# Kernel tuning notes

Hardware: AMD Instinct MI355X
Metric: run time of the kernel (lower is better)

The kernel has to match this reference:

```python
import jax, jax.numpy as jnp
import numpy as np

B, N, DIN, DOUT, E, K = 64, 883, 2, 64, 10, 2
CIN = DIN + DOUT


def _dgcn(x, node_emb, time, day, speed, occupy,
          fc1_w, fc1_b, fc2_w, fc2_b, fc3_w, fc3_b, wpool, bpool):
    # x: (B, N, C); node_emb: (N, E); time/day/speed/occupy: (B, N, E)
    n = x.shape[1]
    # hyper-network filter from input features
    h = jax.nn.sigmoid(x @ fc1_w + fc1_b)
    h = jax.nn.sigmoid(h @ fc2_w + fc2_b)
    filt = h @ fc3_w + fc3_b                                  # (B, N, E)
    # dynamic node embedding: static emb modulated by time/day/speed/occupy embeddings
    dyn = node_emb[None] * time * day * speed * occupy        # (B, N, E)
    nodevec = jnp.tanh(dyn * filt)                            # (B, N, E)
    A = jax.nn.relu(jnp.einsum('bne,bme->bnm', nodevec, nodevec))  # (B, N, N)
    d = jnp.sum(A, axis=-1) ** -0.5                           # (B, N)
    I = jnp.eye(n, dtype=x.dtype)
    L = I[None] - A * d[:, :, None] * d[:, None, :]           # normalized laplacian support
    # cheb_k = 2 supports: identity and L
    x_g = jnp.stack([x, jnp.einsum('bnm,bmc->bnc', L, x)], axis=2)  # (B, N, K, C)
    weights = jnp.einsum('ne,ekio->nkio', node_emb, wpool)    # (N, K, C, O)
    bias = node_emb @ bpool                                   # (N, O)
    return jnp.einsum('bnki,nkio->bno', x_g, weights) + bias[None]


def setup_inputs() -> dict:
    key = jax.random.key(0)
    ks = jax.random.split(key, 23)
    rn = lambda k, s, sc=1.0: jax.random.normal(k, s, dtype=jnp.float32) * sc
    return dict(
        x=rn(ks[0], (B, N, DIN)),
        state=rn(ks[1], (B, N, DOUT), 0.1),
        node_embeddings=rn(ks[2], (N, E)),
        time=rn(ks[3], (B, N, E), 0.5),
        day=rn(ks[4], (B, N, E), 0.5),
        speed=rn(ks[5], (B, N, E), 0.5),
        occupy=rn(ks[6], (B, N, E), 0.5),
        gate_wpool=rn(ks[7], (E, K, CIN, 2 * DOUT), 0.1),
        gate_bpool=rn(ks[8], (E, 2 * DOUT), 0.1),
        gate_fc1_w=rn(ks[9], (CIN, 16), 0.1), gate_fc1_b=rn(ks[10], (16,), 0.1),
        gate_fc2_w=rn(ks[11], (16, 2), 0.1), gate_fc2_b=rn(ks[12], (2,), 0.1),
        gate_fc3_w=rn(ks[13], (2, E), 0.1), gate_fc3_b=rn(ks[14], (E,), 0.1),
        update_wpool=rn(ks[15], (E, K, CIN, DOUT), 0.1),
        update_bpool=rn(ks[16], (E, DOUT), 0.1),
        update_fc1_w=rn(ks[17], (CIN, 16), 0.1), update_fc1_b=rn(ks[18], (16,), 0.1),
        update_fc2_w=rn(ks[19], (16, 2), 0.1), update_fc2_b=rn(ks[20], (2,), 0.1),
        update_fc3_w=rn(ks[21], (2, E), 0.1), update_fc3_b=rn(ks[22], (E,), 0.1),
    )


def reference(x, state, node_embeddings, time, day, speed, occupy,
              gate_wpool, gate_bpool, gate_fc1_w, gate_fc1_b, gate_fc2_w,
              gate_fc2_b, gate_fc3_w, gate_fc3_b,
              update_wpool, update_bpool, update_fc1_w, update_fc1_b,
              update_fc2_w, update_fc2_b, update_fc3_w, update_fc3_b):
    xs = jnp.concatenate([x, state], axis=-1)                 # (B, N, DIN+DOUT)
    z_r = jax.nn.sigmoid(_dgcn(xs, node_embeddings, time, day, speed, occupy,
                               gate_fc1_w, gate_fc1_b, gate_fc2_w, gate_fc2_b,
                               gate_fc3_w, gate_fc3_b, gate_wpool, gate_bpool))
    z, r = jnp.split(z_r, 2, axis=-1)
    cand = jnp.concatenate([x, z * state], axis=-1)
    hc = jnp.tanh(_dgcn(cand, node_embeddings, time, day, speed, occupy,
                        update_fc1_w, update_fc1_b, update_fc2_w, update_fc2_b,
                        update_fc3_w, update_fc3_b, update_wpool, update_bpool))
    return r * state + (1.0 - r) * hc
```

## Files before the change

### kernel.cpp

```cpp
#include <hip/hip_runtime.h>
#include <cmath>

#define BB 64
#define NN 883
#define NP 896
#define EE 10
#define CC 66
#define KP 160
#define NT16 56
#define MB32 28

typedef __attribute__((ext_vector_type(8))) short bf16x8;
typedef __attribute__((ext_vector_type(4))) float f32x4;

__device__ __forceinline__ float sigmoidf_(float v) { return 1.f / (1.f + expf(-v)); }

__device__ __forceinline__ unsigned short f2bf(float f) {
  unsigned int u = __float_as_uint(f);
  u = u + 0x7FFFu + ((u >> 16) & 1u);
  return (unsigned short)(u >> 16);
}
__device__ __forceinline__ float bf2f(unsigned short h) {
  return __uint_as_float(((unsigned int)h) << 16);
}
__device__ __forceinline__ unsigned int pkrelu(float a, float b) {
  return (unsigned int)f2bf(fmaxf(a, 0.f)) | ((unsigned int)f2bf(fmaxf(b, 0.f)) << 16);
}


template<int PHASE>
__global__ __launch_bounds__(256) void k1_hyper(
    const float* __restrict__ x, const float* __restrict__ state,
    const float* __restrict__ zr, const float* __restrict__ emb,
    const float* __restrict__ tme, const float* __restrict__ day,
    const float* __restrict__ spd, const float* __restrict__ occ,
    const float* __restrict__ w1, const float* __restrict__ b1,
    const float* __restrict__ w2, const float* __restrict__ b2,
    const float* __restrict__ w3, const float* __restrict__ b3,
    unsigned short* __restrict__ Acat, unsigned short* __restrict__ nv2) {
  int idx = blockIdx.x * 256 + threadIdx.x;
  if (idx >= BB * NP) return;
  int b = idx / NP, n = idx - b * NP;
  size_t slot = ((size_t)(b * NT16 + (n >> 4)) * 32 + (n & 15) * 2) * 8;
  if (n >= NN) {
    *(uint4*)&nv2[slot] = make_uint4(0, 0, 0, 0);
    *(uint4*)&nv2[slot + 8] = make_uint4(0, 0, 0, 0);
    return;
  }
  int bn = b * NN + n;

  float xsr[CC];
  xsr[0] = x[bn * 2 + 0];
  xsr[1] = x[bn * 2 + 1];
#pragma unroll
  for (int j = 0; j < 64; ++j) {
    float s = state[bn * 64 + j];
    if (PHASE == 1) s *= zr[(size_t)bn * 128 + j];
    xsr[2 + j] = s;
  }
  {
    unsigned short a16[80];
#pragma unroll
    for (int c = 0; c < CC; ++c) a16[c] = f2bf(xsr[c]);
#pragma unroll
    for (int c = CC; c < 80; ++c) a16[c] = 0;
#pragma unroll
    for (int k = 0; k < 10; ++k) {
      unsigned int q0 = (unsigned int)a16[8 * k + 0] | ((unsigned int)a16[8 * k + 1] << 16);
      unsigned int q1 = (unsigned int)a16[8 * k + 2] | ((unsigned int)a16[8 * k + 3] << 16);
      unsigned int q2 = (unsigned int)a16[8 * k + 4] | ((unsigned int)a16[8 * k + 5] << 16);
      unsigned int q3 = (unsigned int)a16[8 * k + 6] | ((unsigned int)a16[8 * k + 7] << 16);
      *(uint4*)&Acat[(size_t)bn * KP + 8 * k] = make_uint4(q0, q1, q2, q3);
    }
  }

  float h1[16];
#pragma unroll
  for (int j = 0; j < 16; ++j) h1[j] = b1[j];
#pragma unroll
  for (int i = 0; i < CC; ++i) {
    float xv = xsr[i];
#pragma unroll
    for (int j = 0; j < 16; ++j) h1[j] = fmaf(xv, w1[i * 16 + j], h1[j]);
  }
#pragma unroll
  for (int j = 0; j < 16; ++j) h1[j] = sigmoidf_(h1[j]);

  float h2[2];
#pragma unroll
  for (int j = 0; j < 2; ++j) {
    float s = b2[j];
#pragma unroll
    for (int i = 0; i < 16; ++i) s = fmaf(h1[i], w2[i * 2 + j], s);
    h2[j] = sigmoidf_(s);
  }

  unsigned short nv16[16];
#pragma unroll
  for (int e = 0; e < EE; ++e) {
    float f = b3[e] + h2[0] * w3[e] + h2[1] * w3[EE + e];
    int be = bn * EE + e;
    float dyn = emb[n * EE + e] * tme[be] * day[be] * spd[be] * occ[be];
    nv16[e] = f2bf(tanhf(dyn * f));
  }
#pragma unroll
  for (int e = EE; e < 16; ++e) nv16[e] = 0;
  unsigned int w[8];
#pragma unroll
  for (int k = 0; k < 8; ++k)
    w[k] = (unsigned int)nv16[2 * k] | ((unsigned int)nv16[2 * k + 1] << 16);
  *(uint4*)&nv2[slot]     = make_uint4(w[0], w[1], w[2], w[3]);
  *(uint4*)&nv2[slot + 8] = make_uint4(w[4], w[5], w[6], w[7]);
}

__global__ __launch_bounds__(256) void k2_deg(const unsigned short* __restrict__ nv2,
                                              const unsigned short* __restrict__ Acat,
                                              float* __restrict__ d_g,
                                              unsigned short* __restrict__ xsd2) {
  int nt = blockIdx.x, b = blockIdx.y;
  int t = threadIdx.x, wid = t >> 6, lane = t & 63;
  int col = lane & 15, q = lane >> 4;
  __shared__ float tile[64][67];
  __shared__ float d_s[64];

  const unsigned short* nvb = nv2 + (size_t)b * NT16 * 32 * 8;
  bf16x8 zf = {0, 0, 0, 0, 0, 0, 0, 0};
  bf16x8 anv = zf;
  if (q < 2) anv = *(const bf16x8*)&nvb[((size_t)(nt * 4 + wid) * 32 + col * 2 + q) * 8];

  float rs[4] = {0.f, 0.f, 0.f, 0.f};
  bf16x8 cur = zf, nxt = zf;
  if (q < 2) cur = *(const bf16x8*)&nvb[((size_t)0 * 32 + col * 2 + q) * 8];
  for (int mt = 0; mt < NT16; ++mt) {
    if (q < 2 && mt + 1 < NT16)
      nxt = *(const bf16x8*)&nvb[((size_t)(mt + 1) * 32 + col * 2 + q) * 8];
    f32x4 z = {0.f, 0.f, 0.f, 0.f};
    f32x4 g = __builtin_amdgcn_mfma_f32_16x16x32_bf16(anv, cur, z, 0, 0, 0);
#pragma unroll
    for (int r = 0; r < 4; ++r) rs[r] += fmaxf(g[r], 0.f);
    cur = nxt;
  }
#pragma unroll
  for (int off = 1; off < 16; off <<= 1) {
#pragma unroll
    for (int r = 0; r < 4; ++r) rs[r] += __shfl_xor(rs[r], off);
  }
  if (col == 0) {
#pragma unroll
    for (int r = 0; r < 4; ++r) {
      int n = nt * 64 + wid * 16 + q * 4 + r;
      float dv = (n < NN) ? rsqrtf(rs[r]) : 0.f;
      d_g[b * NP + n] = dv;
      d_s[wid * 16 + q * 4 + r] = dv;
    }
  }
  __syncthreads();

  int mb = nt * 64;
  for (int idx = t; idx < 64 * CC; idx += 256) {
    int ml = idx / CC, c = idx - ml * CC;
    int m = mb + ml;
    float v = 0.f;
    if (m < NN) v = bf2f(Acat[((size_t)(b * NN + m)) * KP + c]);
    tile[ml][c] = v * d_s[ml];
  }
  __syncthreads();
  for (int idx = t; idx < 2 * 5 * 4 * 16; idx += 256) {
    int colw = idx & 15;
    int qw = (idx >> 4) & 3;
    int ctw = (idx >> 6) % 5;
    int mbbl = idx / (16 * 4 * 5);
    unsigned int o[4];
#pragma unroll
    for (int jj = 0; jj < 4; ++jj) {
      int ml = mbbl * 32 + qw * 8 + jj * 2;
      int c = ctw * 16 + colw;
      float v0 = (c < CC) ? tile[ml][c] : 0.f;
      float v1 = (c < CC) ? tile[ml + 1][c] : 0.f;
      o[jj] = (unsigned int)f2bf(v0) | ((unsigned int)f2bf(v1) << 16);
    }
    size_t dst = (((((size_t)b * MB32 + (nt * 2 + mbbl)) * 5 + ctw) * 4 + qw) * 16 + colw) * 8;
    *(uint4*)&xsd2[dst] = make_uint4(o[0], o[1], o[2], o[3]);
  }
}

__global__ __launch_bounds__(256) void k3_agg(const unsigned short* __restrict__ nv2,
                                              const float* __restrict__ d_g,
                                              const unsigned short* __restrict__ xsd2,
                                              unsigned short* __restrict__ Acat) {
  int nt = blockIdx.x, b = blockIdx.y, t = threadIdx.x;
  int wid = t >> 6, lane = t & 63, col = lane & 15, q = lane >> 4;
  int n16 = nt * 64 + wid * 16;

  const unsigned short* nvb = nv2 + (size_t)b * NT16 * 32 * 8;
  const unsigned short* xb = xsd2 + (size_t)b * MB32 * 5 * 4 * 16 * 8;

  bf16x8 zf = {0, 0, 0, 0, 0, 0, 0, 0};
  bf16x8 anv = zf;
  if (q < 2) anv = *(const bf16x8*)&nvb[((size_t)(nt * 4 + wid) * 32 + col * 2 + q) * 8];

  f32x4 acc[5];
#pragma unroll
  for (int ct = 0; ct < 5; ++ct) acc[ct] = (f32x4){0.f, 0.f, 0.f, 0.f};

  int base = ((q & 1) << 5) + col;
  bool hi = (q >= 2);

  for (int i = 0; i < MB32; ++i) {
    bf16x8 b0 = zf, b1 = zf;
    if (q < 2) {
      b0 = *(const bf16x8*)&nvb[((size_t)(i * 2) * 32 + col * 2 + q) * 8];
      b1 = *(const bf16x8*)&nvb[((size_t)(i * 2 + 1) * 32 + col * 2 + q) * 8];
    }
    bf16x8 xf[5];
#pragma unroll
    for (int ct = 0; ct < 5; ++ct)
      xf[ct] = *(const bf16x8*)&xb[((((size_t)i * 5 + ct) * 4 + q) * 16 + col) * 8];

    f32x4 z = {0.f, 0.f, 0.f, 0.f};
    f32x4 g0 = __builtin_amdgcn_mfma_f32_16x16x32_bf16(b0, anv, z, 0, 0, 0);
    f32x4 g1 = __builtin_amdgcn_mfma_f32_16x16x32_bf16(b1, anv, z, 0, 0, 0);
    unsigned int p00 = pkrelu(g0[0], g0[1]), p01 = pkrelu(g0[2], g0[3]);
    unsigned int p10 = pkrelu(g1[0], g1[1]), p11 = pkrelu(g1[2], g1[3]);
    unsigned int s00 = (unsigned int)__shfl((int)p00, base);
    unsigned int s01 = (unsigned int)__shfl((int)p01, base);
    unsigned int s02 = (unsigned int)__shfl((int)p00, base + 16);
    unsigned int s03 = (unsigned int)__shfl((int)p01, base + 16);
    unsigned int s10 = (unsigned int)__shfl((int)p10, base);
    unsigned int s11 = (unsigned int)__shfl((int)p11, base);
    unsigned int s12 = (unsigned int)__shfl((int)p10, base + 16);
    unsigned int s13 = (unsigned int)__shfl((int)p11, base + 16);
    union { unsigned int u[4]; bf16x8 v; } cv;
    cv.u[0] = hi ? s10 : s00;
    cv.u[1] = hi ? s11 : s01;
    cv.u[2] = hi ? s12 : s02;
    cv.u[3] = hi ? s13 : s03;

#pragma unroll
    for (int ct = 0; ct < 5; ++ct)
      acc[ct] = __builtin_amdgcn_mfma_f32_16x16x32_bf16(cv.v, xf[ct], acc[ct], 0, 0, 0);
  }

  float dn[4];
#pragma unroll
  for (int r = 0; r < 4; ++r) dn[r] = d_g[b * NP + n16 + q * 4 + r];
#pragma unroll
  for (int ct = 0; ct < 5; ++ct) {
    int c = ct * 16 + col;
#pragma unroll
    for (int r = 0; r < 4; ++r) {
      int n = n16 + q * 4 + r;
      if (n < NN)
        Acat[((size_t)(b * NN) + n) * KP + 80 + c] = f2bf(-(acc[ct][r] * dn[r]));
    }
  }
}

template<int OT, bool GATE>
__global__ __launch_bounds__(256) void k4b_gemm(
    const float* __restrict__ emb, const float* __restrict__ wpool,
    const float* __restrict__ bpool, const unsigned short* __restrict__ Acat,
    float* __restrict__ zr_w,
    const float* __restrict__ state, const float* __restrict__ zr_r,
    float* __restrict__ out) {
  int n = blockIdx.x, t = threadIdx.x;
  __shared__ __align__(16) unsigned short Ws[OT * 168];
  __shared__ float bias_s[OT];

  const int OG = OT / 4;
  int og = t % OG, ti = t / OG;
  int o4 = og * 4;
  float em[EE];
#pragma unroll
  for (int e = 0; e < EE; ++e) em[e] = emb[n * EE + e];

  for (int i = ti; i < CC; i += 256 / OG) {
    float4 s0 = make_float4(0.f, 0.f, 0.f, 0.f);
    float4 s1 = make_float4(0.f, 0.f, 0.f, 0.f);
#pragma unroll
    for (int e = 0; e < EE; ++e) {
      float4 w0 = *(const float4*)&wpool[(((size_t)(e * 2 + 0) * CC + i)) * OT + o4];
      float4 w1 = *(const float4*)&wpool[(((size_t)(e * 2 + 1) * CC + i)) * OT + o4];
      s0.x = fmaf(em[e], w0.x, s0.x); s0.y = fmaf(em[e], w0.y, s0.y);
      s0.z = fmaf(em[e], w0.z, s0.z); s0.w = fmaf(em[e], w0.w, s0.w);
      s1.x = fmaf(em[e], w1.x, s1.x); s1.y = fmaf(em[e], w1.y, s1.y);
      s1.z = fmaf(em[e], w1.z, s1.z); s1.w = fmaf(em[e], w1.w, s1.w);
    }
    Ws[(o4 + 0) * 168 + i] = f2bf(s0.x + s1.x);
    Ws[(o4 + 1) * 168 + i] = f2bf(s0.y + s1.y);
    Ws[(o4 + 2) * 168 + i] = f2bf(s0.z + s1.z);
    Ws[(o4 + 3) * 168 + i] = f2bf(s0.w + s1.w);
    Ws[(o4 + 0) * 168 + 80 + i] = f2bf(s1.x);
    Ws[(o4 + 1) * 168 + 80 + i] = f2bf(s1.y);
    Ws[(o4 + 2) * 168 + 80 + i] = f2bf(s1.z);
    Ws[(o4 + 3) * 168 + 80 + i] = f2bf(s1.w);
  }
  for (int idx = t; idx < OT * 14; idx += 256) {
    int o = idx / 14, kk = idx - o * 14;
    Ws[o * 168 + 66 + kk] = 0;
    Ws[o * 168 + 146 + kk] = 0;
  }
  if (t < OT) {
    float s = 0.f;
#pragma unroll
    for (int e = 0; e < EE; ++e) s = fmaf(em[e], bpool[e * OT + t], s);
    bias_s[t] = s;
  }
  __syncthreads();

  int wid = t >> 6, lane = t & 63, col = lane & 15, q = lane >> 4;
  int bA = wid * 16 + col;
  f32x4 acc[OT / 16];
#pragma unroll
  for (int ot = 0; ot < OT / 16; ++ot) acc[ot] = (f32x4){0.f, 0.f, 0.f, 0.f};

#pragma unroll
  for (int ks = 0; ks < 5; ++ks) {
    bf16x8 af = *(const bf16x8*)&Acat[((size_t)(bA * NN + n)) * KP + ks * 32 + q * 8];
#pragma unroll
    for (int ot = 0; ot < OT / 16; ++ot) {
      bf16x8 bf = *(const bf16x8*)&Ws[(ot * 16 + col) * 168 + ks * 32 + q * 8];
      acc[ot] = __builtin_amdgcn_mfma_f32_16x16x32_bf16(af, bf, acc[ot], 0, 0, 0);
    }
  }

#pragma unroll
  for (int ot = 0; ot < OT / 16; ++ot) {
    int o = ot * 16 + col;
    float bia = bias_s[o];
#pragma unroll
    for (int r = 0; r < 4; ++r) {
      int bb = wid * 16 + q * 4 + r;
      float v = acc[ot][r] + bia;
      if (GATE) {
        zr_w[((size_t)(bb * NN + n)) * 128 + o] = sigmoidf_(v);
      } else {
        float hc = tanhf(v);
        float rr = zr_r[((size_t)(bb * NN + n)) * 128 + 64 + o];
        float st = state[((size_t)(bb * NN + n)) * 64 + o];
        out[((size_t)(bb * NN + n)) * 64 + o] = fmaf(rr, st - hc, hc);
      }
    }
  }
}

extern "C" void kernel_launch(void* const* d_in, const int* in_sizes, int n_in,
                              void* d_out, int out_size, void* d_ws, size_t ws_size,
                              hipStream_t stream) {
  const float* x     = (const float*)d_in[0];
  const float* state = (const float*)d_in[1];
  const float* emb   = (const float*)d_in[2];
  const float* tme   = (const float*)d_in[3];
  const float* day   = (const float*)d_in[4];
  const float* spd   = (const float*)d_in[5];
  const float* occ   = (const float*)d_in[6];
  const float* gwp   = (const float*)d_in[7];
  const float* gbp   = (const float*)d_in[8];
  const float* gw1   = (const float*)d_in[9];
  const float* gb1   = (const float*)d_in[10];
  const float* gw2   = (const float*)d_in[11];
  const float* gb2   = (const float*)d_in[12];
  const float* gw3   = (const float*)d_in[13];
  const float* gb3   = (const float*)d_in[14];
  const float* uwp   = (const float*)d_in[15];
  const float* ubp   = (const float*)d_in[16];
  const float* uw1   = (const float*)d_in[17];
  const float* ub1   = (const float*)d_in[18];
  const float* uw2   = (const float*)d_in[19];
  const float* ub2   = (const float*)d_in[20];
  const float* uw3   = (const float*)d_in[21];
  const float* ub3   = (const float*)d_in[22];

  char* w = (char*)d_ws;
  unsigned short* Acat = (unsigned short*)w;  w += (size_t)BB * NN * KP * 2;
  unsigned short* nv2  = (unsigned short*)w;  w += (size_t)BB * NT16 * 32 * 8 * 2;
  unsigned short* xsd2 = (unsigned short*)w;  w += (size_t)BB * MB32 * 5 * 4 * 16 * 8 * 2;
  float* d_g  = (float*)w;  w += (size_t)BB * NP * 4;
  float* zr   = (float*)w;  w += (size_t)BB * NN * 128 * 4;

  dim3 b256(256);
  dim3 gK1((BB * NP) / 256);
  dim3 gK2(14, BB);
  dim3 gK4(NN);

  k1_hyper<0><<<gK1, b256, 0, stream>>>(x, state, zr, emb, tme, day, spd, occ,
                                        gw1, gb1, gw2, gb2, gw3, gb3, Acat, nv2);
  k2_deg<<<gK2, b256, 0, stream>>>(nv2, Acat, d_g, xsd2);
  k3_agg<<<gK2, b256, 0, stream>>>(nv2, d_g, xsd2, Acat);
  k4b_gemm<128, true><<<gK4, b256, 0, stream>>>(emb, gwp, gbp, Acat, zr,
                                                nullptr, nullptr, nullptr);
  k1_hyper<1><<<gK1, b256, 0, stream>>>(x, state, zr, emb, tme, day, spd, occ,
                                        uw1, ub1, uw2, ub2, uw3, ub3, Acat, nv2);
  k2_deg<<<gK2, b256, 0, stream>>>(nv2, Acat, d_g, xsd2);
  k3_agg<<<gK2, b256, 0, stream>>>(nv2, d_g, xsd2, Acat);
  k4b_gemm<64, false><<<gK4, b256, 0, stream>>>(emb, uwp, ubp, Acat, nullptr,
                                                state, zr, (float*)d_out);
}
```

Baseline: 355.1 us.

## Precompute per-node bf16 weights in separate kernel, stream them into GEMM

Adds a k4a_wprep kernel that builds the per-node weights (node_emb x wpool) in bf16, already in MFMA fragment order, into a workspace buffer. The gemm kernel then loads its B fragments straight from global memory and no longer builds them in shared memory with a __syncthreads. The per-node bias is now computed in registers in the epilogue. This takes the redundant per-block weight synthesis and its barrier off the gemm's critical path. The cost is an extra kernel launch and a large global weight buffer (about NN*8*160*16 bf16 elements) that is written and read back.

New measurement: 370.9 us. 4.4% more time.

```diff
diff --git a/kernel.cpp b/kernel.cpp
--- a/kernel.cpp
+++ b/kernel.cpp
@@ -256,78 +256,85 @@
   }
 }
 
+template<int OT>
+__global__ __launch_bounds__(160) void k4a_wprep(const float* __restrict__ emb,
+                                                 const float* __restrict__ wpool,
+                                                 unsigned short* __restrict__ Wg) {
+  const int OTILES = OT / 16;
+  int k = threadIdx.x;
+  int col = blockIdx.x & 15;
+  int ot = blockIdx.x >> 4;
+  int nc = blockIdx.y;
+  int o = ot * 16 + col;
+  int ks = k >> 5, qw = (k >> 3) & 3, j = k & 7;
+
+  int i = -1, half = 0;
+  if (k < CC) { i = k; half = 0; }
+  else if (k >= 80 && k < 80 + CC) { i = k - 80; half = 1; }
+
+  float wv[EE];
+#pragma unroll
+  for (int e = 0; e < EE; ++e) {
+    float v = 0.f;
+    if (i >= 0) {
+      v = wpool[(((size_t)(e * 2 + 1) * CC + i)) * OT + o];
+      if (half == 0) v += wpool[(((size_t)(e * 2 + 0) * CC + i)) * OT + o];
+    }
+    wv[e] = v;
+  }
+
+  __shared__ float emb_s[112 * EE];
+  int n0 = nc * 111;
+  int cnt = min(111, NN - n0);
+  for (int idx = k; idx < cnt * EE; idx += 160) emb_s[idx] = emb[n0 * EE + idx];
+  __syncthreads();
+
+  size_t wo = (((size_t)ot * 5 + ks) * 4 + qw) * 16 * 8 + col * 8 + j;
+  for (int nl = 0; nl < cnt; ++nl) {
+    float s = 0.f;
+#pragma unroll
+    for (int e = 0; e < EE; ++e) s = fmaf(emb_s[nl * EE + e], wv[e], s);
+    Wg[(size_t)(n0 + nl) * (OTILES * KP * 16) + wo] = f2bf(s);
+  }
+}
+
 template<int OT, bool GATE>
 __global__ __launch_bounds__(256) void k4b_gemm(
-    const float* __restrict__ emb, const float* __restrict__ wpool,
+    const float* __restrict__ emb, const unsigned short* __restrict__ Wg,
     const float* __restrict__ bpool, const unsigned short* __restrict__ Acat,
     float* __restrict__ zr_w,
     const float* __restrict__ state, const float* __restrict__ zr_r,
     float* __restrict__ out) {
+  const int OTILES = OT / 16;
   int n = blockIdx.x, t = threadIdx.x;
-  __shared__ __align__(16) unsigned short Ws[OT * 168];
-  __shared__ float bias_s[OT];
-
-  const int OG = OT / 4;
-  int og = t % OG, ti = t / OG;
-  int o4 = og * 4;
-  float em[EE];
-#pragma unroll
-  for (int e = 0; e < EE; ++e) em[e] = emb[n * EE + e];
-
-  for (int i = ti; i < CC; i += 256 / OG) {
-    float4 s0 = make_float4(0.f, 0.f, 0.f, 0.f);
-    float4 s1 = make_float4(0.f, 0.f, 0.f, 0.f);
-#pragma unroll
-    for (int e = 0; e < EE; ++e) {
-      float4 w0 = *(const float4*)&wpool[(((size_t)(e * 2 + 0) * CC + i)) * OT + o4];
-      float4 w1 = *(const float4*)&wpool[(((size_t)(e * 2 + 1) * CC + i)) * OT + o4];
-      s0.x = fmaf(em[e], w0.x, s0.x); s0.y = fmaf(em[e], w0.y, s0.y);
-      s0.z = fmaf(em[e], w0.z, s0.z); s0.w = fmaf(em[e], w0.w, s0.w);
-      s1.x = fmaf(em[e], w1.x, s1.x); s1.y = fmaf(em[e], w1.y, s1.y);
-      s1.z = fmaf(em[e], w1.z, s1.z); s1.w = fmaf(em[e], w1.w, s1.w);
-    }
-    Ws[(o4 + 0) * 168 + i] = f2bf(s0.x + s1.x);
-    Ws[(o4 + 1) * 168 + i] = f2bf(s0.y + s1.y);
-    Ws[(o4 + 2) * 168 + i] = f2bf(s0.z + s1.z);
-    Ws[(o4 + 3) * 168 + i] = f2bf(s0.w + s1.w);
-    Ws[(o4 + 0) * 168 + 80 + i] = f2bf(s1.x);
-    Ws[(o4 + 1) * 168 + 80 + i] = f2bf(s1.y);
-    Ws[(o4 + 2) * 168 + 80 + i] = f2bf(s1.z);
-    Ws[(o4 + 3) * 168 + 80 + i] = f2bf(s1.w);
-  }
-  for (int idx = t; idx < OT * 14; idx += 256) {
-    int o = idx / 14, kk = idx - o * 14;
-    Ws[o * 168 + 66 + kk] = 0;
-    Ws[o * 168 + 146 + kk] = 0;
-  }
-  if (t < OT) {
-    float s = 0.f;
-#pragma unroll
-    for (int e = 0; e < EE; ++e) s = fmaf(em[e], bpool[e * OT + t], s);
-    bias_s[t] = s;
-  }
-  __syncthreads();
-
   int wid = t >> 6, lane = t & 63, col = lane & 15, q = lane >> 4;
   int bA = wid * 16 + col;
-  f32x4 acc[OT / 16];
-#pragma unroll
-  for (int ot = 0; ot < OT / 16; ++ot) acc[ot] = (f32x4){0.f, 0.f, 0.f, 0.f};
+  const unsigned short* wb = Wg + (size_t)n * (OTILES * KP * 16);
+
+  f32x4 acc[OTILES];
+#pragma unroll
+  for (int ot = 0; ot < OTILES; ++ot) acc[ot] = (f32x4){0.f, 0.f, 0.f, 0.f};
 
 #pragma unroll
   for (int ks = 0; ks < 5; ++ks) {
     bf16x8 af = *(const bf16x8*)&Acat[((size_t)(bA * NN + n)) * KP + ks * 32 + q * 8];
 #pragma unroll
-    for (int ot = 0; ot < OT / 16; ++ot) {
-      bf16x8 bf = *(const bf16x8*)&Ws[(ot * 16 + col) * 168 + ks * 32 + q * 8];
+    for (int ot = 0; ot < OTILES; ++ot) {
+      bf16x8 bf = *(const bf16x8*)&wb[((((size_t)ot * 5 + ks) * 4 + q) * 16 + col) * 8];
       acc[ot] = __builtin_amdgcn_mfma_f32_16x16x32_bf16(af, bf, acc[ot], 0, 0, 0);
     }
   }
 
-#pragma unroll
-  for (int ot = 0; ot < OT / 16; ++ot) {
+  float em[EE];
+#pragma unroll
+  for (int e = 0; e < EE; ++e) em[e] = emb[n * EE + e];
+
+#pragma unroll
+  for (int ot = 0; ot < OTILES; ++ot) {
     int o = ot * 16 + col;
-    float bia = bias_s[o];
+    float bia = 0.f;
+#pragma unroll
+    for (int e = 0; e < EE; ++e) bia = fmaf(em[e], bpool[e * OT + o], bia);
 #pragma unroll
     for (int r = 0; r < 4; ++r) {
       int bb = wid * 16 + q * 4 + r;
@@ -377,22 +384,26 @@
   unsigned short* xsd2 = (unsigned short*)w;  w += (size_t)BB * MB32 * 5 * 4 * 16 * 8 * 2;
   float* d_g  = (float*)w;  w += (size_t)BB * NP * 4;
   float* zr   = (float*)w;  w += (size_t)BB * NN * 128 * 4;
-
-  dim3 b256(256);
+  unsigned short* Wg = (unsigned short*)w;  w += (size_t)NN * 8 * KP * 16 * 2;
+
+  dim3 b256(256), b160(160);
   dim3 gK1((BB * NP) / 256);
   dim3 gK2(14, BB);
   dim3 gK4(NN);
-
+  dim3 gWg(8 * 16, 8), gWu(4 * 16, 8);
+
+  k4a_wprep<128><<<gWg, b160, 0, stream>>>(emb, gwp, Wg);
   k1_hyper<0><<<gK1, b256, 0, stream>>>(x, state, zr, emb, tme, day, spd, occ,
                                         gw1, gb1, gw2, gb2, gw3, gb3, Acat, nv2);
   k2_deg<<<gK2, b256, 0, stream>>>(nv2, Acat, d_g, xsd2);
   k3_agg<<<gK2, b256, 0, stream>>>(nv2, d_g, xsd2, Acat);
-  k4b_gemm<128, true><<<gK4, b256, 0, stream>>>(emb, gwp, gbp, Acat, zr,
+  k4b_gemm<128, true><<<gK4, b256, 0, stream>>>(emb, Wg, gbp, Acat, zr,
                                                 nullptr, nullptr, nullptr);
+  k4a_wprep<64><<<gWu, b160, 0, stream>>>(emb, uwp, Wg);
   k1_hyper<1><<<gK1, b256, 0, stream>>>(x, state, zr, emb, tme, day, spd, occ,
                                         uw1, ub1, uw2, ub2, uw3, ub3, Acat, nv2);
   k2_deg<<<gK2, b256, 0, stream>>>(nv2, Acat, d_g, xsd2);
   k3_agg<<<gK2, b256, 0, stream>>>(nv2, d_g, xsd2, Acat);
-  k4b_gemm<64, false><<<gK4, b256, 0, stream>>>(emb, uwp, ubp, Acat, nullptr,
+  k4b_gemm<64, false><<<gK4, b256, 0, stream>>>(emb, Wg, ubp, Acat, nullptr,
                                                 state, zr, (float*)d_out);
 }
```
